# Kernel tuning notes

Measured on AMD Instinct MI355X. Metric: run time of the kernel, lower is better.

The kernel has to match this reference:

```python
import jax, jax.numpy as jnp
import numpy as np

E, H, L, B = 2048, 32, 1024, 4
S = E // H  # 64
DM, DD = 32, 64


def _ln(x, w, b, eps=1e-5):
    m = x.mean(-1, keepdims=True)
    v = ((x - m) ** 2).mean(-1, keepdims=True)
    return (x - m) / jnp.sqrt(v + eps) * w + b


def setup_inputs() -> dict:
    key = jax.random.key(0)
    ks = jax.random.split(key, 24)
    sc = 0.02  # weight scale for stability
    d = {
        'x': jax.random.normal(ks[0], (B, L, E), jnp.float32),
        'state': jax.random.normal(ks[1], (B, 2 + S, E), jnp.float32) * 0.1,
        'ln1_w': jnp.ones((E,), jnp.float32), 'ln1_b': jnp.zeros((E,), jnp.float32),
        'ln2_w': jnp.ones((E,), jnp.float32), 'ln2_b': jnp.zeros((E,), jnp.float32),
        'maa_x': jax.random.normal(ks[2], (E,), jnp.float32) * 0.1,
        'maa_w1': jax.random.normal(ks[3], (E, 5 * DM), jnp.float32) * sc,
        'maa_w2': jax.random.normal(ks[4], (5, DM, E), jnp.float32) * sc,
        'maa_stack': jax.random.normal(ks[5], (1, 5, E), jnp.float32) * 0.1,
        'time_decay': jax.random.normal(ks[6], (E,), jnp.float32) * 0.5,
        'td_w1': jax.random.normal(ks[7], (E, DD), jnp.float32) * sc,
        'td_w2': jax.random.normal(ks[8], (DD, E), jnp.float32) * sc,
        'u': jax.random.normal(ks[9], (H, S, 1), jnp.float32) * 0.1,
        'Wr': jax.random.normal(ks[10], (E, E), jnp.float32) * sc,
        'Wk': jax.random.normal(ks[11], (E, E), jnp.float32) * sc,
        'Wv': jax.random.normal(ks[12], (E, E), jnp.float32) * sc,
        'Wg': jax.random.normal(ks[13], (E, E), jnp.float32) * sc,
        'Wo': jax.random.normal(ks[14], (E, E), jnp.float32) * sc,
        'gn_w': jnp.ones((E,), jnp.float32), 'gn_b': jnp.zeros((E,), jnp.float32),
        'ffn_maa_k': jax.random.normal(ks[15], (E,), jnp.float32) * 0.1,
        'ffn_maa_r': jax.random.normal(ks[16], (E,), jnp.float32) * 0.1,
        'Wfk': jax.random.normal(ks[17], (E, E), jnp.float32) * sc,
        'Wfr': jax.random.normal(ks[18], (E, E), jnp.float32) * sc,
        'Wfv': jax.random.normal(ks[19], (E, E), jnp.float32) * sc,
    }
    return d


def _block(x, state, ln1_w, ln1_b, ln2_w, ln2_b, maa_x, maa_w1, maa_w2, maa_stack,
           time_decay, td_w1, td_w2, u, Wr, Wk, Wv, Wg, Wo, gn_w, gn_b,
           ffn_maa_k, ffn_maa_r, Wfk, Wfr, Wfv):
    b, l, e = x.shape
    h = u.shape[0]
    s_ = e // h
    # ---- time mixing (parallel over L, sequential WKV scan) ----
    xa = _ln(x, ln1_w, ln1_b)
    # token shift: sx[t] = x[t-1] - x[t], seeded from state row 1
    sx = jnp.concatenate([state[:, 1:2] - xa[:, :1], xa[:, :-1] - xa[:, 1:]], axis=1)
    xxx = jnp.tanh((xa + sx * maa_x) @ maa_w1).reshape(b, l, 5, DM)
    xxx = jnp.einsum('blfd,fde->blfe', xxx, maa_w2)            # [B,L,5,E]
    xm = xa[:, :, None] + sx[:, :, None] * (maa_stack + xxx)   # [B,L,5,E]
    xk, xw, xv, xr, xg = (xm[:, :, j] for j in range(5))       # stack order: k,w,v,r,g
    w = jnp.exp(-jnp.exp(time_decay + jnp.tanh(xw @ td_w1) @ td_w2)).reshape(b, l, h, s_)
    r = (xr @ Wr.T).reshape(b, l, h, s_)
    k = (xk @ Wk.T).reshape(b, l, h, s_)
    v = (xv @ Wv.T).reshape(b, l, h, s_)
    g = jax.nn.silu(xg @ Wg.T)                                 # [B,L,E]
    s0 = state[:, 2:2 + s_].reshape(b, h, s_, s_)              # per-head WKV state

    def step(s, rkvw):
        r_t, k_t, v_t, w_t = rkvw                              # each [B,H,S]
        a = k_t[..., :, None] * v_t[..., None, :]              # outer product [B,H,S,S]
        out = jnp.einsum('bhi,bhij->bhj', r_t, u * a + s)      # [B,H,S]
        s = a + w_t[..., :, None] * s
        return s, out

    rkvw = tuple(jnp.moveaxis(t, 1, 0) for t in (r, k, v, w))  # [L,B,H,S]
    _, out = jax.lax.scan(step, s0, rkvw)
    out = jnp.moveaxis(out, 0, 1).reshape(b, l, e)             # [B,L,E]
    # group norm over heads (eps=1e-5)
    og = out.reshape(b, l, h, s_)
    m = og.mean(-1, keepdims=True)
    va = ((og - m) ** 2).mean(-1, keepdims=True)
    og = ((og - m) / jnp.sqrt(va + 1e-5)).reshape(b, l, e) * gn_w + gn_b
    x1 = x + (og * g) @ Wo.T
    # ---- channel mixing ----
    xc = _ln(x1, ln2_w, ln2_b)
    sx2 = jnp.concatenate([state[:, 0:1] - xc[:, :1], xc[:, :-1] - xc[:, 1:]], axis=1)
    xk2 = xc + sx2 * ffn_maa_k
    xr2 = xc + sx2 * ffn_maa_r
    rr = jax.nn.sigmoid(xr2 @ Wfr.T)
    kk = jnp.square(jax.nn.relu(xk2 @ Wfk.T))
    return x1 + rr * (kk @ Wfv.T)


def reference(x, state, ln1_w, ln1_b, ln2_w, ln2_b, maa_x, maa_w1, maa_w2, maa_stack,
              time_decay, td_w1, td_w2, u, Wr, Wk, Wv, Wg, Wo, gn_w, gn_b,
              ffn_maa_k, ffn_maa_r, Wfk, Wfr, Wfv):
    return _block(x, state, ln1_w, ln1_b, ln2_w, ln2_b, maa_x, maa_w1, maa_w2, maa_stack,
                  time_decay, td_w1, td_w2, u, Wr, Wk, Wv, Wg, Wo, gn_w, gn_b,
                  ffn_maa_k, ffn_maa_r, Wfk, Wfr, Wfv)
```

## Files before the change

kernel.cpp:

```cpp
#include <hip/hip_runtime.h>


#define E     2048
#define LL    1024
#define HHH   32
#define SSS   64
#define NBL   4096
#define NBLE  8388608

typedef short bf16x8 __attribute__((ext_vector_type(8)));
typedef float f32x4  __attribute__((ext_vector_type(4)));
using u16 = unsigned short;

__device__ __forceinline__ u16 f2b(float f) {
    union { float f; unsigned int u; } c; c.f = f;
    unsigned int u = c.u;
    unsigned int r = (u + 0x7fffu + ((u >> 16) & 1u)) >> 16;
    return (u16)r;
}
__device__ __forceinline__ float b2f(u16 b) {
    union { unsigned int u; float f; } c; c.u = ((unsigned int)b) << 16; return c.f;
}

__device__ __forceinline__ float wave_sum(float v) {
#pragma unroll
    for (int m = 32; m >= 1; m >>= 1) v += __shfl_xor(v, m, 64);
    return v;
}

__device__ __forceinline__ void gl_lds16(const void* g, void* l) {
    __builtin_amdgcn_global_load_lds((const __attribute__((address_space(1))) unsigned int*)g,
                                     (__attribute__((address_space(3))) unsigned int*)l, 16, 0, 0);
}


__global__ __launch_bounds__(256) void k_convert(const float* __restrict__ in,
                                                 u16* __restrict__ out, int n) {
    int i = (blockIdx.x * 256 + threadIdx.x) * 4;
    if (i >= n) return;
    float4 v = *reinterpret_cast<const float4*>(in + i);
    ushort4 o = make_ushort4(f2b(v.x), f2b(v.y), f2b(v.z), f2b(v.w));
    *reinterpret_cast<ushort4*>(out + i) = o;
}

__global__ __launch_bounds__(256) void k_transpose(const float* __restrict__ in,
                                                   u16* __restrict__ out, int R, int C) {
    int i = blockIdx.x * 256 + threadIdx.x;
    if (i >= R * C) return;
    int r = i / C, c = i - r * C;
    out[c * R + r] = f2b(in[i]);
}

__global__ __launch_bounds__(256) void k_ln(const float* __restrict__ x,
                                            const float* __restrict__ w,
                                            const float* __restrict__ b,
                                            float* __restrict__ out) {
    int row = blockIdx.x, tid = threadIdx.x;
    const float* xr = x + (size_t)row * E + tid * 8;
    float4 v0 = *reinterpret_cast<const float4*>(xr);
    float4 v1 = *reinterpret_cast<const float4*>(xr + 4);
    float s = v0.x + v0.y + v0.z + v0.w + v1.x + v1.y + v1.z + v1.w;
    __shared__ float red[4];
    s = wave_sum(s);
    int wid = tid >> 6, lane = tid & 63;
    if (lane == 0) red[wid] = s;
    __syncthreads();
    float mean = (red[0] + red[1] + red[2] + red[3]) * (1.0f / E);
    __syncthreads();
    float q = 0.f;
    q += (v0.x - mean) * (v0.x - mean); q += (v0.y - mean) * (v0.y - mean);
    q += (v0.z - mean) * (v0.z - mean); q += (v0.w - mean) * (v0.w - mean);
    q += (v1.x - mean) * (v1.x - mean); q += (v1.y - mean) * (v1.y - mean);
    q += (v1.z - mean) * (v1.z - mean); q += (v1.w - mean) * (v1.w - mean);
    q = wave_sum(q);
    if (lane == 0) red[wid] = q;
    __syncthreads();
    float inv = rsqrtf((red[0] + red[1] + red[2] + red[3]) * (1.0f / E) + 1e-5f);
    int e = tid * 8;
    float4 w0 = *reinterpret_cast<const float4*>(w + e);
    float4 w1 = *reinterpret_cast<const float4*>(w + e + 4);
    float4 b0 = *reinterpret_cast<const float4*>(b + e);
    float4 b1 = *reinterpret_cast<const float4*>(b + e + 4);
    float4 o0, o1;
    o0.x = (v0.x - mean) * inv * w0.x + b0.x; o0.y = (v0.y - mean) * inv * w0.y + b0.y;
    o0.z = (v0.z - mean) * inv * w0.z + b0.z; o0.w = (v0.w - mean) * inv * w0.w + b0.w;
    o1.x = (v1.x - mean) * inv * w1.x + b1.x; o1.y = (v1.y - mean) * inv * w1.y + b1.y;
    o1.z = (v1.z - mean) * inv * w1.z + b1.z; o1.w = (v1.w - mean) * inv * w1.w + b1.w;
    float* op = out + (size_t)row * E + e;
    *reinterpret_cast<float4*>(op) = o0;
    *reinterpret_cast<float4*>(op + 4) = o1;
}

__global__ __launch_bounds__(256) void k_mk(const float* __restrict__ xa,
                                            const float* __restrict__ state,
                                            const float* __restrict__ maa_x,
                                            u16* __restrict__ out) {
    int i = (blockIdx.x * 256 + threadIdx.x) * 4;
    if (i >= NBLE) return;
    int n = i >> 11, e = i & (E - 1);
    int l = n & (LL - 1), b = n >> 10;
    float4 cur = *reinterpret_cast<const float4*>(xa + i);
    float4 prev;
    if (l > 0) prev = *reinterpret_cast<const float4*>(xa + i - E);
    else       prev = *reinterpret_cast<const float4*>(state + (size_t)b * 66 * E + E + e);
    float4 m = *reinterpret_cast<const float4*>(maa_x + e);
    ushort4 o = make_ushort4(f2b(cur.x + (prev.x - cur.x) * m.x),
                             f2b(cur.y + (prev.y - cur.y) * m.y),
                             f2b(cur.z + (prev.z - cur.z) * m.z),
                             f2b(cur.w + (prev.w - cur.w) * m.w));
    *reinterpret_cast<ushort4*>(out + i) = o;
}

__global__ __launch_bounds__(256) void k_mix2(const float* __restrict__ xc,
                                              const float* __restrict__ state,
                                              const float* __restrict__ mk,
                                              const float* __restrict__ mr,
                                              u16* __restrict__ xk2,
                                              u16* __restrict__ xr2) {
    int i = (blockIdx.x * 256 + threadIdx.x) * 4;
    if (i >= NBLE) return;
    int n = i >> 11, e = i & (E - 1);
    int l = n & (LL - 1), b = n >> 10;
    float4 cur = *reinterpret_cast<const float4*>(xc + i);
    float4 prev;
    if (l > 0) prev = *reinterpret_cast<const float4*>(xc + i - E);
    else       prev = *reinterpret_cast<const float4*>(state + (size_t)b * 66 * E + e);
    float4 sx = make_float4(prev.x - cur.x, prev.y - cur.y, prev.z - cur.z, prev.w - cur.w);
    float4 k4 = *reinterpret_cast<const float4*>(mk + e);
    float4 r4 = *reinterpret_cast<const float4*>(mr + e);
    ushort4 ok = make_ushort4(f2b(cur.x + sx.x * k4.x), f2b(cur.y + sx.y * k4.y),
                              f2b(cur.z + sx.z * k4.z), f2b(cur.w + sx.w * k4.w));
    ushort4 orr = make_ushort4(f2b(cur.x + sx.x * r4.x), f2b(cur.y + sx.y * r4.y),
                               f2b(cur.z + sx.z * r4.z), f2b(cur.w + sx.w * r4.w));
    *reinterpret_cast<ushort4*>(xk2 + i) = ok;
    *reinterpret_cast<ushort4*>(xr2 + i) = orr;
}

__global__ __launch_bounds__(256) void k_gnorm(const float* __restrict__ wkv,
                                               const u16* __restrict__ g,
                                               const float* __restrict__ gw,
                                               const float* __restrict__ gb,
                                               u16* __restrict__ ogg) {
    int gidx = blockIdx.x * 4 + (threadIdx.x >> 6);
    int lane = threadIdx.x & 63;
    int n = gidx >> 5, h = gidx & 31;
    size_t base = (size_t)n * E + h * SSS;
    float v = wkv[base + lane];
    float mean = wave_sum(v) * (1.0f / SSS);
    float d = v - mean;
    float var = wave_sum(d * d) * (1.0f / SSS);
    float norm = d * rsqrtf(var + 1e-5f);
    int e = h * SSS + lane;
    float res = norm * gw[e] + gb[e];
    float gv = b2f(g[base + lane]);
    ogg[base + lane] = f2b(res * gv);
}

#define CT 16

__global__ __launch_bounds__(256) void k_scan(const u16* __restrict__ Rb,
                                              const u16* __restrict__ Kb,
                                              const u16* __restrict__ Vb,
                                              const float* __restrict__ W,
                                              const float* __restrict__ state,
                                              const float* __restrict__ u,
                                              float* __restrict__ out) {
    __shared__ u16   ldsR[2][CT * 64];
    __shared__ u16   ldsK[2][CT * 64];
    __shared__ float ldsW[2][CT * 64];
    __shared__ u16   ldsV[2][CT * 16];
    const int blk = blockIdx.x;
    const int bh = blk & 127;
    const int jq = blk >> 7;
    const int b = bh >> 5, h = bh & 31;
    const int tid = threadIdx.x;
    const int wvid = tid >> 6;
    const int lane = tid & 63;
    const int ig = lane >> 2;
    const int jl = lane & 3;
    const int jv = wvid * 4 + jl;
    const int j  = jq * 16 + jv;
    const int i0 = ig * 4;
    float s[4], uu[4];
    const float* s0 = state + (size_t)b * 66 * E + 2 * E + h * (SSS * SSS);
#pragma unroll
    for (int ii = 0; ii < 4; ii++) {
        s[ii] = s0[(i0 + ii) * SSS + j];
        uu[ii] = u[h * SSS + i0 + ii];
    }
    const size_t off0 = (size_t)b * LL * E + h * SSS;

    auto stage = [&](int c, int bufsel) {
        size_t base = off0 + (size_t)c * CT * E;
        if (wvid == 0) {
            const u16* g0 = Rb + base + (size_t)(lane >> 3) * E + ((lane & 7) << 3);
            gl_lds16(g0,         &ldsR[bufsel][lane * 8]);
            gl_lds16(g0 + 8 * E, &ldsR[bufsel][512 + lane * 8]);
            if (lane < 32) {
                const u16* gv = Vb + base + (size_t)(lane >> 1) * E + jq * 16 + ((lane & 1) << 3);
                gl_lds16(gv, &ldsV[bufsel][lane * 8]);
            }
        } else if (wvid == 1) {
            const u16* g0 = Kb + base + (size_t)(lane >> 3) * E + ((lane & 7) << 3);
            gl_lds16(g0,         &ldsK[bufsel][lane * 8]);
            gl_lds16(g0 + 8 * E, &ldsK[bufsel][512 + lane * 8]);
        } else if (wvid == 2) {
            const float* g0 = W + base + (size_t)(lane >> 4) * E + ((lane & 15) << 2);
            gl_lds16(g0,         &ldsW[bufsel][lane * 4]);
            gl_lds16(g0 + 4 * E, &ldsW[bufsel][256 + lane * 4]);
        } else {
            const float* g0 = W + base + (size_t)(8 + (lane >> 4)) * E + ((lane & 15) << 2);
            gl_lds16(g0,         &ldsW[bufsel][512 + lane * 4]);
            gl_lds16(g0 + 4 * E, &ldsW[bufsel][768 + lane * 4]);
        }
    };

    stage(0, 0);
    __syncthreads();
    int cur = 0;
    for (int c = 0; c < LL / CT; c++) {
        if (c + 1 < LL / CT) stage(c + 1, cur ^ 1);
        float accs[CT];
#pragma unroll
        for (int tt = 0; tt < CT; tt++) {
            ushort4 rv = *reinterpret_cast<const ushort4*>(&ldsR[cur][tt * 64 + i0]);
            ushort4 kv = *reinterpret_cast<const ushort4*>(&ldsK[cur][tt * 64 + i0]);
            float4  wv = *reinterpret_cast<const float4*>(&ldsW[cur][tt * 64 + i0]);
            float vj = b2f(ldsV[cur][tt * 16 + jv]);
            float acc = 0.f, a;
            a = b2f(kv.x) * vj; acc += b2f(rv.x) * fmaf(uu[0], a, s[0]); s[0] = fmaf(wv.x, s[0], a);
            a = b2f(kv.y) * vj; acc += b2f(rv.y) * fmaf(uu[1], a, s[1]); s[1] = fmaf(wv.y, s[1], a);
            a = b2f(kv.z) * vj; acc += b2f(rv.z) * fmaf(uu[2], a, s[2]); s[2] = fmaf(wv.z, s[2], a);
            a = b2f(kv.w) * vj; acc += b2f(rv.w) * fmaf(uu[3], a, s[3]); s[3] = fmaf(wv.w, s[3], a);
            accs[tt] = acc;
        }
#pragma unroll
        for (int tt = 0; tt < CT; tt++) accs[tt] += __shfl_xor(accs[tt], 4, 64);
#pragma unroll
        for (int tt = 0; tt < CT; tt++) accs[tt] += __shfl_xor(accs[tt], 8, 64);
#pragma unroll
        for (int tt = 0; tt < CT; tt++) accs[tt] += __shfl_xor(accs[tt], 16, 64);
#pragma unroll
        for (int tt = 0; tt < CT; tt++) accs[tt] += __shfl_xor(accs[tt], 32, 64);
        if (ig == 0) {
            size_t offt = off0 + (size_t)c * CT * E + j;
#pragma unroll
            for (int tt = 0; tt < CT; tt++) out[offt + (size_t)tt * E] = accs[tt];
        }
        __syncthreads();
        cur ^= 1;
    }
}

template <int EP>
__global__ __launch_bounds__(512, 2) void k_gemm256(const u16* __restrict__ A,
                                                    const u16* __restrict__ Bw,
                                                    void* __restrict__ C,
                                                    const float* __restrict__ emat1,
                                                    const float* __restrict__ emat2) {
    __shared__ u16 As[2][256 * 64];
    __shared__ u16 Bs[2][128 * 64];
    const int tid = threadIdx.x;
    const int bid = blockIdx.x;
    const int sw = (bid & 7) * 32 + (bid >> 3);
    const int m0 = (sw >> 4) << 8;
    const int n0 = (sw & 15) << 7;
    const int srow = tid >> 3;
    const int schunk = (tid & 7) ^ (srow & 7);
    const u16* gA = A + (size_t)(m0 + srow) * E + schunk * 8;
    const u16* gB = Bw + (size_t)(n0 + srow) * E + schunk * 8;
    u16* lA = &As[0][0] + tid * 8;
    u16* lB = &Bs[0][0] + tid * 8;

    const int wv = tid >> 6, lane = tid & 63;
    const int wm = wv >> 2, wn = wv & 3;
    const int lr = lane & 15, lq = lane >> 4;
    const int c0 = ((lq ^ (lr & 7)) << 3);
    const int c1 = (((4 + lq) ^ (lr & 7)) << 3);
    const int arow = wm * 128 + lr;
    const int brow = wn * 32 + lr;

    f32x4 acc[8][2];
#pragma unroll
    for (int mt = 0; mt < 8; mt++)
#pragma unroll
        for (int nt = 0; nt < 2; nt++) acc[mt][nt] = {0.f, 0.f, 0.f, 0.f};

    auto stage = [&](int kt, int buf) {
        const u16* a = gA + kt * 64;
        const u16* b = gB + kt * 64;
        u16* la = lA + buf * (256 * 64);
        u16* lb = lB + buf * (128 * 64);
        gl_lds16(a,                 la);
        gl_lds16(a + (size_t)64  * E, la + 64 * 64);
        gl_lds16(a + (size_t)128 * E, la + 128 * 64);
        gl_lds16(a + (size_t)192 * E, la + 192 * 64);
        gl_lds16(b,                 lb);
        gl_lds16(b + (size_t)64  * E, lb + 64 * 64);
    };

    stage(0, 0);
    int cur = 0;
    for (int kt = 0; kt < E / 64; kt++) {
        if (kt + 1 < E / 64) {
            stage(kt + 1, cur ^ 1);
            asm volatile("s_waitcnt vmcnt(6)" ::: "memory");
        } else {
            asm volatile("s_waitcnt vmcnt(0)" ::: "memory");
        }
        __builtin_amdgcn_s_barrier();
        const u16* as = &As[0][0] + cur * (256 * 64);
        const u16* bs = &Bs[0][0] + cur * (128 * 64);
        bf16x8 af0[8], af1[8], bf0[2], bf1[2];
#pragma unroll
        for (int mt = 0; mt < 8; mt++) {
            af0[mt] = *reinterpret_cast<const bf16x8*>(as + (arow + mt * 16) * 64 + c0);
            af1[mt] = *reinterpret_cast<const bf16x8*>(as + (arow + mt * 16) * 64 + c1);
        }
#pragma unroll
        for (int nt = 0; nt < 2; nt++) {
            bf0[nt] = *reinterpret_cast<const bf16x8*>(bs + (brow + nt * 16) * 64 + c0);
            bf1[nt] = *reinterpret_cast<const bf16x8*>(bs + (brow + nt * 16) * 64 + c1);
        }
        asm volatile("s_waitcnt lgkmcnt(0)" ::: "memory");
        __builtin_amdgcn_s_barrier();
        __builtin_amdgcn_s_setprio(1);
#pragma unroll
        for (int mt = 0; mt < 8; mt++) {
#pragma unroll
            for (int nt = 0; nt < 2; nt++) {
                acc[mt][nt] = __builtin_amdgcn_mfma_f32_16x16x32_bf16(af0[mt], bf0[nt], acc[mt][nt], 0, 0, 0);
                acc[mt][nt] = __builtin_amdgcn_mfma_f32_16x16x32_bf16(af1[mt], bf1[nt], acc[mt][nt], 0, 0, 0);
            }
        }
        __builtin_amdgcn_s_setprio(0);
        cur ^= 1;
    }

    const int gmb = m0 + wm * 128 + (lq << 2);
    const int gnb = n0 + wn * 32 + lr;
#pragma unroll
    for (int mt = 0; mt < 8; mt++) {
#pragma unroll
        for (int nt = 0; nt < 2; nt++) {
            int gn = gnb + nt * 16;
#pragma unroll
            for (int i = 0; i < 4; i++) {
                int gm = gmb + mt * 16 + i;
                size_t idx = (size_t)gm * E + gn;
                float v = acc[mt][nt][i];
                if constexpr (EP == 5) ((float*)C)[idx] = emat1[idx] + v;
                else if constexpr (EP == 6) ((float*)C)[idx] = 1.f / (1.f + expf(-v));
                else if constexpr (EP == 7) { float t = fmaxf(v, 0.f); ((u16*)C)[idx] = f2b(t * t); }
                else if constexpr (EP == 8) ((float*)C)[idx] = emat1[idx] + emat2[idx] * v;
                else if constexpr (EP == 9) ((u16*)C)[idx] = f2b(v);
                else if constexpr (EP == 10) { float sg = 1.f / (1.f + expf(-v)); ((u16*)C)[idx] = f2b(v * sg); }
            }
        }
    }
}

template <int EP>
__global__ __launch_bounds__(256) void k_gemm128(const u16* __restrict__ A, int lda,
                                                 const u16* __restrict__ Bw,
                                                 void* __restrict__ C, int K,
                                                 const float* __restrict__ evec,
                                                 const float* __restrict__ emat1,
                                                 const float* __restrict__ emat2) {
    __shared__ u16 As[128 * 32];
    __shared__ u16 Bs[128 * 32];
    const int tid = threadIdx.x;
    const int m0 = blockIdx.y << 7, n0 = blockIdx.x << 7;
    const int srow = tid >> 2;
    const int scol = (((tid & 3) ^ ((srow >> 1) & 3)) << 3);
    const int wv = tid >> 6, lane = tid & 63;
    const int wy = (wv >> 1) << 6, wx = (wv & 1) << 6;
    const int lr = lane & 15, lq = lane >> 4;
    const int cofs = ((lq ^ ((lr >> 1) & 3)) << 3);
    f32x4 acc[4][4];
#pragma unroll
    for (int a = 0; a < 4; a++)
#pragma unroll
        for (int bq = 0; bq < 4; bq++) acc[a][bq] = {0.f, 0.f, 0.f, 0.f};
    const u16* gA = A + (size_t)(m0 + srow) * lda + scol;
    const u16* gB = Bw + (size_t)(n0 + srow) * K + scol;
    u16* lA = As + srow * 32 + ((tid & 3) << 3);
    u16* lB = Bs + srow * 32 + ((tid & 3) << 3);
    for (int k0 = 0; k0 < K; k0 += 32) {
        gl_lds16(gA + k0, lA);
        gl_lds16(gA + (size_t)64 * lda + k0, lA + 64 * 32);
        gl_lds16(gB + k0, lB);
        gl_lds16(gB + (size_t)64 * K + k0, lB + 64 * 32);
        __syncthreads();
        bf16x8 af[4], bfr[4];
#pragma unroll
        for (int mt = 0; mt < 4; mt++)
            af[mt] = *reinterpret_cast<const bf16x8*>(As + (wy + mt * 16 + lr) * 32 + cofs);
#pragma unroll
        for (int nt = 0; nt < 4; nt++)
            bfr[nt] = *reinterpret_cast<const bf16x8*>(Bs + (wx + nt * 16 + lr) * 32 + cofs);
#pragma unroll
        for (int mt = 0; mt < 4; mt++)
#pragma unroll
            for (int nt = 0; nt < 4; nt++)
                acc[mt][nt] = __builtin_amdgcn_mfma_f32_16x16x32_bf16(af[mt], bfr[nt], acc[mt][nt], 0, 0, 0);
        __syncthreads();
    }
    const int gmb = m0 + wy + (lq << 2);
    const int gnb = n0 + wx + lr;
#pragma unroll
    for (int mt = 0; mt < 4; mt++) {
#pragma unroll
        for (int nt = 0; nt < 4; nt++) {
            int gn = gnb + nt * 16;
#pragma unroll
            for (int i = 0; i < 4; i++) {
                int gm = gmb + mt * 16 + i;
                size_t idx = (size_t)gm * E + gn;
                float v = acc[mt][nt][i];
                if constexpr (EP == 2) {
                    int l = gm & (LL - 1), bb = gm >> 10;
                    float cur = emat1[idx];
                    float prev = (l > 0) ? emat1[idx - E]
                                         : emat2[(size_t)bb * 66 * E + E + gn];
                    ((u16*)C)[idx] = f2b(cur + (prev - cur) * (evec[gn] + v));
                }
                else if constexpr (EP == 3) ((float*)C)[idx] = expf(-expf(evec[gn] + v));
            }
        }
    }
}

#define BK  32
#define LDP 40

template <int EP>
__global__ __launch_bounds__(256) void k_gemm(const u16* __restrict__ A, int lda,
                                              const u16* __restrict__ Bw,
                                              void* __restrict__ C,
                                              int M, int N, int K) {
    __shared__ u16 As[64 * LDP];
    __shared__ u16 Bs[64 * LDP];
    const int tid = threadIdx.x;
    const int m0 = blockIdx.y << 6, n0 = blockIdx.x << 6;
    const int srow = tid >> 2, skc = (tid & 3) << 3;
    const int lane = tid & 63, wv = tid >> 6;
    const int wr = (wv >> 1) << 5, wc = (wv & 1) << 5;
    const int lr = lane & 15, lq = lane >> 4;
    f32x4 acc[2][2];
#pragma unroll
    for (int a = 0; a < 2; a++)
#pragma unroll
        for (int bq = 0; bq < 2; bq++) acc[a][bq] = {0.f, 0.f, 0.f, 0.f};
    const u16* aptr = A + (size_t)(m0 + srow) * lda + skc;
    const u16* bptr = Bw + (size_t)(n0 + srow) * K + skc;
    const bool bvalid = (n0 + srow) < N;
    for (int k0 = 0; k0 < K; k0 += BK) {
        float4 av = *reinterpret_cast<const float4*>(aptr + k0);
        float4 bv = bvalid ? *reinterpret_cast<const float4*>(bptr + k0)
                           : make_float4(0.f, 0.f, 0.f, 0.f);
        __syncthreads();
        *reinterpret_cast<float4*>(As + srow * LDP + skc) = av;
        *reinterpret_cast<float4*>(Bs + srow * LDP + skc) = bv;
        __syncthreads();
        bf16x8 a0 = *reinterpret_cast<const bf16x8*>(As + (wr + lr) * LDP + lq * 8);
        bf16x8 a1 = *reinterpret_cast<const bf16x8*>(As + (wr + 16 + lr) * LDP + lq * 8);
        bf16x8 b0 = *reinterpret_cast<const bf16x8*>(Bs + (wc + lr) * LDP + lq * 8);
        bf16x8 b1 = *reinterpret_cast<const bf16x8*>(Bs + (wc + 16 + lr) * LDP + lq * 8);
        acc[0][0] = __builtin_amdgcn_mfma_f32_16x16x32_bf16(a0, b0, acc[0][0], 0, 0, 0);
        acc[0][1] = __builtin_amdgcn_mfma_f32_16x16x32_bf16(a0, b1, acc[0][1], 0, 0, 0);
        acc[1][0] = __builtin_amdgcn_mfma_f32_16x16x32_bf16(a1, b0, acc[1][0], 0, 0, 0);
        acc[1][1] = __builtin_amdgcn_mfma_f32_16x16x32_bf16(a1, b1, acc[1][1], 0, 0, 0);
    }
    const int gmb = m0 + wr + lq * 4;
    const int gnb = n0 + wc + lr;
#pragma unroll
    for (int mi = 0; mi < 2; mi++) {
#pragma unroll
        for (int ni = 0; ni < 2; ni++) {
            int gn = gnb + ni * 16;
            if (gn >= N) continue;
#pragma unroll
            for (int i = 0; i < 4; i++) {
                int gm = gmb + mi * 16 + i;
                size_t idx = (size_t)gm * N + gn;
                float v = acc[mi][ni][i];
                if constexpr (EP == 1) ((u16*)C)[idx] = f2b(tanhf(v));
            }
        }
    }
}


extern "C" void kernel_launch(void* const* d_in, const int* in_sizes, int n_in,
                              void* d_out, int out_size, void* d_ws, size_t ws_size,
                              hipStream_t stream) {
    const float* x          = (const float*)d_in[0];
    const float* state      = (const float*)d_in[1];
    const float* ln1_w      = (const float*)d_in[2];
    const float* ln1_b      = (const float*)d_in[3];
    const float* ln2_w      = (const float*)d_in[4];
    const float* ln2_b      = (const float*)d_in[5];
    const float* maa_x      = (const float*)d_in[6];
    const float* maa_w1     = (const float*)d_in[7];
    const float* maa_w2     = (const float*)d_in[8];
    const float* maa_stack  = (const float*)d_in[9];
    const float* time_decay = (const float*)d_in[10];
    const float* td_w1      = (const float*)d_in[11];
    const float* td_w2      = (const float*)d_in[12];
    const float* u          = (const float*)d_in[13];
    const float* Wr         = (const float*)d_in[14];
    const float* Wk         = (const float*)d_in[15];
    const float* Wv         = (const float*)d_in[16];
    const float* Wg         = (const float*)d_in[17];
    const float* Wo         = (const float*)d_in[18];
    const float* gn_w       = (const float*)d_in[19];
    const float* gn_b       = (const float*)d_in[20];
    const float* ffn_k      = (const float*)d_in[21];
    const float* ffn_r      = (const float*)d_in[22];
    const float* Wfk        = (const float*)d_in[23];
    const float* Wfr        = (const float*)d_in[24];
    const float* Wfv        = (const float*)d_in[25];

    char* ws = (char*)d_ws;
    float* R0 = (float*)(ws);
    float* R1 = (float*)(ws + 33554432);
    u16*   R2 = (u16*)(ws + 67108864);
    u16*   R3 = (u16*)(ws + 83886080);
    u16*   R4 = (u16*)(ws + 100663296);
    u16*   R5 = (u16*)(ws + 117440512);
    u16*   R6 = (u16*)(ws + 134217728);
    u16*   WB = (u16*)(ws + 150994944);
    u16*   Hx = (u16*)(ws + 159383552);
    u16*   Ht = (u16*)(ws + 160694272);
    u16*  WT1 = (u16*)(ws + 161218560);
    u16*  WT2 = (u16*)(ws + 161873920);
    u16*  WT3 = (u16*)(ws + 162529280);
    u16*  WT4 = (u16*)(ws + 162791424);

    dim3 blk(256);
    dim3 blk512(512);
    dim3 g256(256);
    dim3 g128(16, 32);
    dim3 g160(3, 64), g64(1, 64);
    const int ncv = (E * E / 4) / 256;
    const int nel = NBLE / 1024;

    k_transpose<<<(E * 160 + 255) / 256, blk, 0, stream>>>(maa_w1, WT1, E, 160);
    for (int f = 0; f < 5; f++)
        k_transpose<<<(32 * E + 255) / 256, blk, 0, stream>>>(maa_w2 + f * 32 * E, WT2 + f * E * 32, 32, E);
    k_transpose<<<(E * 64 + 255) / 256, blk, 0, stream>>>(td_w1, WT3, E, 64);
    k_transpose<<<(64 * E + 255) / 256, blk, 0, stream>>>(td_w2, WT4, 64, E);

    k_ln<<<NBL, blk, 0, stream>>>(x, ln1_w, ln1_b, R0);
    k_mk<<<nel, blk, 0, stream>>>(R0, state, maa_x, R2);
    k_gemm<1><<<g160, blk, 0, stream>>>(R2, E, WT1, Hx, NBL, 160, E);

    k_gemm128<2><<<g128, blk, 0, stream>>>(Hx + 1 * 32, 160, WT2 + 1 * E * 32, R2, 32,
                                           maa_stack + 1 * E, R0, state);
    k_gemm<1><<<g64, blk, 0, stream>>>(R2, E, WT3, Ht, NBL, 64, E);
    k_gemm128<3><<<g128, blk, 0, stream>>>(Ht, 64, WT4, R1, 64, time_decay, nullptr, nullptr);

    k_gemm128<2><<<g128, blk, 0, stream>>>(Hx + 0 * 32, 160, WT2 + 0 * E * 32, R2, 32,
                                           maa_stack + 0 * E, R0, state);
    k_convert<<<ncv, blk, 0, stream>>>(Wk, WB, E * E);
    k_gemm256<9><<<g256, blk512, 0, stream>>>(R2, WB, R4, nullptr, nullptr);

    k_gemm128<2><<<g128, blk, 0, stream>>>(Hx + 2 * 32, 160, WT2 + 2 * E * 32, R2, 32,
                                           maa_stack + 2 * E, R0, state);
    k_convert<<<ncv, blk, 0, stream>>>(Wv, WB, E * E);
    k_gemm256<9><<<g256, blk512, 0, stream>>>(R2, WB, R5, nullptr, nullptr);

    k_gemm128<2><<<g128, blk, 0, stream>>>(Hx + 4 * 32, 160, WT2 + 4 * E * 32, R2, 32,
                                           maa_stack + 4 * E, R0, state);
    k_convert<<<ncv, blk, 0, stream>>>(Wg, WB, E * E);
    k_gemm256<10><<<g256, blk512, 0, stream>>>(R2, WB, R6, nullptr, nullptr);

    k_gemm128<2><<<g128, blk, 0, stream>>>(Hx + 3 * 32, 160, WT2 + 3 * E * 32, R2, 32,
                                           maa_stack + 3 * E, R0, state);
    k_convert<<<ncv, blk, 0, stream>>>(Wr, WB, E * E);
    k_gemm256<9><<<g256, blk512, 0, stream>>>(R2, WB, R3, nullptr, nullptr);

    k_scan<<<512, blk, 0, stream>>>(R3, R4, R5, R1, state, u, R0);
    k_gnorm<<<NBL * HHH / 4, blk, 0, stream>>>(R0, R6, gn_w, gn_b, R6);

    k_convert<<<ncv, blk, 0, stream>>>(Wo, WB, E * E);
    k_gemm256<5><<<g256, blk512, 0, stream>>>(R6, WB, R0, x, nullptr);

    k_ln<<<NBL, blk, 0, stream>>>(R0, ln2_w, ln2_b, R1);
    k_mix2<<<nel, blk, 0, stream>>>(R1, state, ffn_k, ffn_r, R2, R3);
    k_convert<<<ncv, blk, 0, stream>>>(Wfk, WB, E * E);
    k_gemm256<7><<<g256, blk512, 0, stream>>>(R2, WB, R4, nullptr, nullptr);
    k_convert<<<ncv, blk, 0, stream>>>(Wfr, WB, E * E);
    k_gemm256<6><<<g256, blk512, 0, stream>>>(R3, WB, R1, nullptr, nullptr);
    k_convert<<<ncv, blk, 0, stream>>>(Wfv, WB, E * E);
    k_gemm256<8><<<g256, blk512, 0, stream>>>(R4, WB, (float*)d_out, R0, R1);
}
```

Baseline: 1.145 ms.

## Triple-buffer GEMM256 and interleave split global loads with MFMA phases

Measured after the change: 1.035 ms. 9.6% less time.

```diff
diff --git a/kernel.cpp b/kernel.cpp
--- a/kernel.cpp
+++ b/kernel.cpp
@@ -258,8 +258,8 @@
                                                     void* __restrict__ C,
                                                     const float* __restrict__ emat1,
                                                     const float* __restrict__ emat2) {
-    __shared__ u16 As[2][256 * 64];
-    __shared__ u16 Bs[2][128 * 64];
+    __shared__ u16 As[3][256 * 64];
+    __shared__ u16 Bs[3][128 * 64];
     const int tid = threadIdx.x;
     const int bid = blockIdx.x;
     const int sw = (bid & 7) * 32 + (bid >> 3);
@@ -269,80 +269,123 @@
     const int schunk = (tid & 7) ^ (srow & 7);
     const u16* gA = A + (size_t)(m0 + srow) * E + schunk * 8;
     const u16* gB = Bw + (size_t)(n0 + srow) * E + schunk * 8;
-    u16* lA = &As[0][0] + tid * 8;
-    u16* lB = &Bs[0][0] + tid * 8;
 
     const int wv = tid >> 6, lane = tid & 63;
-    const int wm = wv >> 2, wn = wv & 3;
+    const int wm = wv >> 1, wn = wv & 1;
     const int lr = lane & 15, lq = lane >> 4;
     const int c0 = ((lq ^ (lr & 7)) << 3);
     const int c1 = (((4 + lq) ^ (lr & 7)) << 3);
-    const int arow = wm * 128 + lr;
-    const int brow = wn * 32 + lr;
-
-    f32x4 acc[8][2];
-#pragma unroll
-    for (int mt = 0; mt < 8; mt++)
-#pragma unroll
-        for (int nt = 0; nt < 2; nt++) acc[mt][nt] = {0.f, 0.f, 0.f, 0.f};
-
-    auto stage = [&](int kt, int buf) {
+    const int arow = wm * 64 + lr;
+    const int brow = wn * 64 + lr;
+
+    f32x4 acc[4][4];
+#pragma unroll
+    for (int mt = 0; mt < 4; mt++)
+#pragma unroll
+        for (int nt = 0; nt < 4; nt++) acc[mt][nt] = {0.f, 0.f, 0.f, 0.f};
+
+    const int NT = E / 64;
+
+    auto stage_full = [&](int kt, int buf) {
         const u16* a = gA + kt * 64;
         const u16* b = gB + kt * 64;
-        u16* la = lA + buf * (256 * 64);
-        u16* lb = lB + buf * (128 * 64);
-        gl_lds16(a,                 la);
+        u16* la = &As[buf][0] + tid * 8;
+        u16* lb = &Bs[buf][0] + tid * 8;
+        gl_lds16(a,                   la);
         gl_lds16(a + (size_t)64  * E, la + 64 * 64);
         gl_lds16(a + (size_t)128 * E, la + 128 * 64);
         gl_lds16(a + (size_t)192 * E, la + 192 * 64);
-        gl_lds16(b,                 lb);
+        gl_lds16(b,                   lb);
         gl_lds16(b + (size_t)64  * E, lb + 64 * 64);
     };
 
-    stage(0, 0);
-    int cur = 0;
-    for (int kt = 0; kt < E / 64; kt++) {
-        if (kt + 1 < E / 64) {
-            stage(kt + 1, cur ^ 1);
-            asm volatile("s_waitcnt vmcnt(6)" ::: "memory");
-        } else {
-            asm volatile("s_waitcnt vmcnt(0)" ::: "memory");
-        }
-        __builtin_amdgcn_s_barrier();
-        const u16* as = &As[0][0] + cur * (256 * 64);
-        const u16* bs = &Bs[0][0] + cur * (128 * 64);
-        bf16x8 af0[8], af1[8], bf0[2], bf1[2];
-#pragma unroll
-        for (int mt = 0; mt < 8; mt++) {
-            af0[mt] = *reinterpret_cast<const bf16x8*>(as + (arow + mt * 16) * 64 + c0);
-            af1[mt] = *reinterpret_cast<const bf16x8*>(as + (arow + mt * 16) * 64 + c1);
-        }
-#pragma unroll
-        for (int nt = 0; nt < 2; nt++) {
-            bf0[nt] = *reinterpret_cast<const bf16x8*>(bs + (brow + nt * 16) * 64 + c0);
-            bf1[nt] = *reinterpret_cast<const bf16x8*>(bs + (brow + nt * 16) * 64 + c1);
-        }
+    stage_full(0, 0);
+    stage_full(1, 1);
+    asm volatile("s_waitcnt vmcnt(6)" ::: "memory");
+    __builtin_amdgcn_s_barrier();
+
+    for (int kt = 0; kt < NT; kt++) {
+        const int rb = kt % 3;
+        const int sb = (kt + 2) % 3;
+        const bool st = (kt + 2) < NT;
+        const u16* as = &As[rb][0];
+        const u16* bs = &Bs[rb][0];
+        const u16* ga = gA + (kt + 2) * 64;
+        const u16* gb = gB + (kt + 2) * 64;
+        u16* la = &As[sb][0] + tid * 8;
+        u16* lb = &Bs[sb][0] + tid * 8;
+        bf16x8 a0, a1, b0[4], b1[4];
+
+        a0 = *reinterpret_cast<const bf16x8*>(as + (arow +  0) * 64 + c0);
+        a1 = *reinterpret_cast<const bf16x8*>(as + (arow + 16) * 64 + c0);
+#pragma unroll
+        for (int nt = 0; nt < 4; nt++)
+            b0[nt] = *reinterpret_cast<const bf16x8*>(bs + (brow + nt * 16) * 64 + c0);
+        if (st) { gl_lds16(ga, la); gl_lds16(ga + (size_t)64 * E, la + 64 * 64); }
+        __builtin_amdgcn_s_barrier();
         asm volatile("s_waitcnt lgkmcnt(0)" ::: "memory");
-        __builtin_amdgcn_s_barrier();
         __builtin_amdgcn_s_setprio(1);
 #pragma unroll
-        for (int mt = 0; mt < 8; mt++) {
-#pragma unroll
-            for (int nt = 0; nt < 2; nt++) {
-                acc[mt][nt] = __builtin_amdgcn_mfma_f32_16x16x32_bf16(af0[mt], bf0[nt], acc[mt][nt], 0, 0, 0);
-                acc[mt][nt] = __builtin_amdgcn_mfma_f32_16x16x32_bf16(af1[mt], bf1[nt], acc[mt][nt], 0, 0, 0);
-            }
+        for (int nt = 0; nt < 4; nt++) {
+            acc[0][nt] = __builtin_amdgcn_mfma_f32_16x16x32_bf16(a0, b0[nt], acc[0][nt], 0, 0, 0);
+            acc[1][nt] = __builtin_amdgcn_mfma_f32_16x16x32_bf16(a1, b0[nt], acc[1][nt], 0, 0, 0);
         }
         __builtin_amdgcn_s_setprio(0);
-        cur ^= 1;
-    }
-
-    const int gmb = m0 + wm * 128 + (lq << 2);
-    const int gnb = n0 + wn * 32 + lr;
-#pragma unroll
-    for (int mt = 0; mt < 8; mt++) {
-#pragma unroll
-        for (int nt = 0; nt < 2; nt++) {
+        __builtin_amdgcn_s_barrier();
+
+        a0 = *reinterpret_cast<const bf16x8*>(as + (arow +  0) * 64 + c1);
+        a1 = *reinterpret_cast<const bf16x8*>(as + (arow + 16) * 64 + c1);
+#pragma unroll
+        for (int nt = 0; nt < 4; nt++)
+            b1[nt] = *reinterpret_cast<const bf16x8*>(bs + (brow + nt * 16) * 64 + c1);
+        if (st) { gl_lds16(ga + (size_t)128 * E, la + 128 * 64); gl_lds16(ga + (size_t)192 * E, la + 192 * 64); }
+        __builtin_amdgcn_s_barrier();
+        asm volatile("s_waitcnt lgkmcnt(0)" ::: "memory");
+        __builtin_amdgcn_s_setprio(1);
+#pragma unroll
+        for (int nt = 0; nt < 4; nt++) {
+            acc[0][nt] = __builtin_amdgcn_mfma_f32_16x16x32_bf16(a0, b1[nt], acc[0][nt], 0, 0, 0);
+            acc[1][nt] = __builtin_amdgcn_mfma_f32_16x16x32_bf16(a1, b1[nt], acc[1][nt], 0, 0, 0);
+        }
+        __builtin_amdgcn_s_setprio(0);
+        __builtin_amdgcn_s_barrier();
+
+        a0 = *reinterpret_cast<const bf16x8*>(as + (arow + 32) * 64 + c0);
+        a1 = *reinterpret_cast<const bf16x8*>(as + (arow + 48) * 64 + c0);
+        if (st) { gl_lds16(gb, lb); gl_lds16(gb + (size_t)64 * E, lb + 64 * 64); }
+        __builtin_amdgcn_s_barrier();
+        asm volatile("s_waitcnt lgkmcnt(0)" ::: "memory");
+        __builtin_amdgcn_s_setprio(1);
+#pragma unroll
+        for (int nt = 0; nt < 4; nt++) {
+            acc[2][nt] = __builtin_amdgcn_mfma_f32_16x16x32_bf16(a0, b0[nt], acc[2][nt], 0, 0, 0);
+            acc[3][nt] = __builtin_amdgcn_mfma_f32_16x16x32_bf16(a1, b0[nt], acc[3][nt], 0, 0, 0);
+        }
+        __builtin_amdgcn_s_setprio(0);
+        __builtin_amdgcn_s_barrier();
+
+        a0 = *reinterpret_cast<const bf16x8*>(as + (arow + 32) * 64 + c1);
+        a1 = *reinterpret_cast<const bf16x8*>(as + (arow + 48) * 64 + c1);
+        if (st) asm volatile("s_waitcnt vmcnt(6)" ::: "memory");
+        else    asm volatile("s_waitcnt vmcnt(0)" ::: "memory");
+        __builtin_amdgcn_s_barrier();
+        asm volatile("s_waitcnt lgkmcnt(0)" ::: "memory");
+        __builtin_amdgcn_s_setprio(1);
+#pragma unroll
+        for (int nt = 0; nt < 4; nt++) {
+            acc[2][nt] = __builtin_amdgcn_mfma_f32_16x16x32_bf16(a0, b1[nt], acc[2][nt], 0, 0, 0);
+            acc[3][nt] = __builtin_amdgcn_mfma_f32_16x16x32_bf16(a1, b1[nt], acc[3][nt], 0, 0, 0);
+        }
+        __builtin_amdgcn_s_setprio(0);
+        __builtin_amdgcn_s_barrier();
+    }
+
+    const int gmb = m0 + wm * 64 + (lq << 2);
+    const int gnb = n0 + wn * 64 + lr;
+#pragma unroll
+    for (int mt = 0; mt < 4; mt++) {
+#pragma unroll
+        for (int nt = 0; nt < 4; nt++) {
             int gn = gnb + nt * 16;
 #pragma unroll
             for (int i = 0; i < 4; i++) {
```
